# Optimization experiments

Measured on AMD Instinct MI355X. Metric: run time of the kernel, lower is better.

## Reference

```python
import jax, jax.numpy as jnp
import numpy as np

HIDDEN = 256
DEPTH = 3
MOL_ATOMS = 42  # padding_final_size in MPNEncoder.padding (AM_dim0=False)
ATOM_FDIM = 133
BOND_FDIM = 147
N_MOLS = 4000
N_ATOMS = N_MOLS * MOL_ATOMS
N_BONDS = 360000
MAX_NB = 6


def setup_inputs() -> dict:
    key = jax.random.key(0)
    ks = jax.random.split(key, 9)
    f_atoms = jax.random.normal(ks[0], (N_ATOMS, ATOM_FDIM), dtype=jnp.float32)
    f_bonds = jax.random.normal(ks[1], (N_BONDS, BOND_FDIM), dtype=jnp.float32)
    a2b = jax.random.randint(ks[2], (N_ATOMS, MAX_NB), 0, N_BONDS, dtype=jnp.int32)
    b2a = jax.random.randint(ks[3], (N_BONDS,), 0, N_ATOMS, dtype=jnp.int32)
    b2revb = jax.random.randint(ks[4], (N_BONDS,), 0, N_BONDS, dtype=jnp.int32)
    # learned params (bias=False for W_i/W_h, W_o has bias, per chemprop defaults)
    W_i = jax.random.normal(ks[5], (HIDDEN, BOND_FDIM), dtype=jnp.float32) * 0.05
    W_h = jax.random.normal(ks[6], (HIDDEN, HIDDEN), dtype=jnp.float32) * 0.05
    W_o = jax.random.normal(ks[7], (HIDDEN, ATOM_FDIM + HIDDEN), dtype=jnp.float32) * 0.05
    b_o = jax.random.normal(ks[8], (HIDDEN,), dtype=jnp.float32) * 0.05
    return dict(f_atoms=f_atoms, f_bonds=f_bonds, W_i=W_i, W_h=W_h, W_o=W_o,
                b_o=b_o, a2b=a2b, b2a=b2a, b2revb=b2revb)


def reference(f_atoms, f_bonds, W_i, W_h, W_o, b_o, a2b, b2a, b2revb):
    # bond-message MPN (atom_messages=False, undirected=False, dropout=0)
    relu = jax.nn.relu
    inp = f_bonds @ W_i.T                         # [n_bonds, H]
    message = relu(inp)

    def atom_hidden(a_msg):
        a_input = jnp.concatenate([f_atoms, a_msg], axis=1)  # [n_atoms, fa+H]
        return relu(a_input @ W_o.T + b_o)

    # depth-0 hidden: a_input = [f_atoms, zeros(H)] (the 'padding' tensor)
    save_depth = [atom_hidden(jnp.zeros((f_atoms.shape[0], HIDDEN), f_atoms.dtype))]
    for d in range(DEPTH - 1):
        if d == 0:
            save_depth.append(atom_hidden(message[a2b].sum(axis=1)))
        a_message = message[a2b].sum(axis=1)      # gather+sum over neighbors
        message = a_message[b2a] - message[b2revb]
        message = relu(inp + message @ W_h.T)
        save_depth.append(atom_hidden(message[a2b].sum(axis=1)))

    # every molecule has exactly MOL_ATOMS atoms -> padding() is identity,
    # per-molecule narrow/stack becomes a reshape
    def pool(h):
        return h.reshape(N_MOLS, MOL_ATOMS, HIDDEN)

    d0, d1, d2 = pool(save_depth[0]), pool(save_depth[1]), pool(save_depth[2])
    dfin = pool(save_depth[-1])
    mol_vecs = dfin.mean(axis=1)                  # sum / a_size
    return (d0, d1, d2, dfin, mol_vecs)
```

## Files before the change

kernel.cpp:

```cpp
#include <hip/hip_runtime.h>

typedef unsigned short u16;
typedef unsigned int u32;
typedef __bf16 bf16x8 __attribute__((ext_vector_type(8)));
typedef float f32x4 __attribute__((ext_vector_type(4)));

__device__ __forceinline__ float bf2f(u16 h) {
  union { u32 u; float f; } c; c.u = ((u32)h) << 16; return c.f;
}
__device__ __forceinline__ float bflo(u32 u) {
  union { u32 u; float f; } c; c.u = u << 16; return c.f;
}
__device__ __forceinline__ float bfhi(u32 u) {
  union { u32 u; float f; } c; c.u = u & 0xffff0000u; return c.f;
}
__device__ __forceinline__ u32 pack2bf(float a, float b) {
  union { __bf16 h[2]; u32 u; } c; c.h[0] = (__bf16)a; c.h[1] = (__bf16)b;
  return c.u;
}
__device__ __forceinline__ u16 f2bf(float f) {
  union { __bf16 h; u16 u; } c; c.h = (__bf16)f; return c.u;
}
__device__ __forceinline__ float relu(float x) { return x > 0.f ? x : 0.f; }

__global__ __launch_bounds__(256) void cvt_w(const float* __restrict__ src,
                                             u16* __restrict__ dst, int N,
                                             int Ks, int Kd, int src_stride,
                                             int col0) {
  int i = blockIdx.x * 256 + threadIdx.x;
  if (i >= N * Kd) return;
  int n = i / Kd, k = i % Kd;
  float v = (k < Ks) ? src[(size_t)n * src_stride + col0 + k] : 0.f;
  dst[i] = f2bf(v);
}

template <int ASRC, int EPI, int KPAD>
__global__ __launch_bounds__(256, 3) void gemm5(
    const float* __restrict__ Af, int Kreal,
    const u16* __restrict__ Ab, const u16* __restrict__ Ab2,
    const int* __restrict__ idx1, const int* __restrict__ idx2,
    const u16* __restrict__ Bw,
    const u16* __restrict__ addb, const float* __restrict__ bias,
    u16* __restrict__ outb0, float* __restrict__ outf) {
  constexpr int LDK = KPAD + 8;
  __shared__ u16 As[64 * LDK];

  const int tid = threadIdx.x;
  const int lane = tid & 63;
  const int wn = (tid >> 6) * 64;
  const int m0 = blockIdx.x * 64;
  const int lm = lane & 15, lg = lane >> 4;
  const int koff = lg * 8;

  if constexpr (ASRC == 0) {
#pragma unroll
    for (int p = 0; p < 64 * KPAD / 512; ++p) {
      int e = (p * 256 + tid) * 2;
      int row = e / KPAD, k = e % KPAD;
      const float* src = Af + (size_t)(m0 + row) * Kreal + k;
      float x0 = (k < Kreal) ? src[0] : 0.f;
      float x1 = (k + 1 < Kreal) ? src[1] : 0.f;
      *reinterpret_cast<u32*>(&As[row * LDK + k]) = pack2bf(x0, x1);
    }
  } else if constexpr (ASRC == 1) {
#pragma unroll
    for (int p = 0; p < 64 * KPAD / 8 / 256; ++p) {
      int ch = p * 256 + tid;
      int row = ch / (KPAD / 8), c8 = ch % (KPAD / 8);
      uint4 v = *reinterpret_cast<const uint4*>(Ab + (size_t)(m0 + row) * KPAD + c8 * 8);
      *reinterpret_cast<uint4*>(&As[row * LDK + c8 * 8]) = v;
    }
  } else {
    static_assert(KPAD == 256, "ASRC2 assumes KPAD=256");
    const int row = tid >> 2, seg = tid & 3;
    const int gr = m0 + row;
    const int r1 = idx1[gr], r2 = idx2[gr];
    const u16* pa = Ab + (size_t)r1 * KPAD + seg * 64;
    const u16* pb = Ab2 + (size_t)r2 * KPAD + seg * 64;
    uint4 va[8], vb[8];
#pragma unroll
    for (int i = 0; i < 8; ++i) va[i] = *reinterpret_cast<const uint4*>(pa + i * 8);
#pragma unroll
    for (int i = 0; i < 8; ++i) vb[i] = *reinterpret_cast<const uint4*>(pb + i * 8);
    u16* dst = &As[row * LDK + seg * 64];
#pragma unroll
    for (int i = 0; i < 8; ++i) {
      uint4 o;
      o.x = pack2bf(bflo(va[i].x) - relu(bflo(vb[i].x)),
                    bfhi(va[i].x) - relu(bfhi(vb[i].x)));
      o.y = pack2bf(bflo(va[i].y) - relu(bflo(vb[i].y)),
                    bfhi(va[i].y) - relu(bfhi(vb[i].y)));
      o.z = pack2bf(bflo(va[i].z) - relu(bflo(vb[i].z)),
                    bfhi(va[i].z) - relu(bfhi(vb[i].z)));
      o.w = pack2bf(bflo(va[i].w) - relu(bflo(vb[i].w)),
                    bfhi(va[i].w) - relu(bfhi(vb[i].w)));
      *reinterpret_cast<uint4*>(dst + i * 8) = o;
    }
  }
  __syncthreads();

  f32x4 acc[4][4];
#pragma unroll
  for (int i = 0; i < 4; ++i)
#pragma unroll
    for (int j = 0; j < 4; ++j) acc[i][j] = (f32x4)(0.f);

#pragma unroll
  for (int kk = 0; kk < KPAD / 32; ++kk) {
    const int k0 = kk * 32 + koff;
    bf16x8 a[4];
#pragma unroll
    for (int im = 0; im < 4; ++im)
      a[im] = *reinterpret_cast<const bf16x8*>(&As[(im * 16 + lm) * LDK + k0]);
#pragma unroll
    for (int jw = 0; jw < 4; ++jw) {
      bf16x8 b = *reinterpret_cast<const bf16x8*>(
          Bw + (size_t)(wn + jw * 16 + lm) * KPAD + k0);
#pragma unroll
      for (int im = 0; im < 4; ++im)
        acc[im][jw] = __builtin_amdgcn_mfma_f32_16x16x32_bf16(b, a[im], acc[im][jw], 0, 0, 0);
    }
  }

#pragma unroll
  for (int im = 0; im < 4; ++im) {
#pragma unroll
    for (int jw = 0; jw < 4; ++jw) {
      const int r = m0 + im * 16 + lm;
      const int c0 = wn + jw * 16 + lg * 4;
      const size_t idx = (size_t)r * 256 + c0;
      f32x4 v = acc[im][jw];
      if constexpr (EPI == 0) {
        uint2 o; o.x = pack2bf(v[0], v[1]); o.y = pack2bf(v[2], v[3]);
        *reinterpret_cast<uint2*>(outb0 + idx) = o;
      } else if constexpr (EPI == 1) {
        const float4 bb = *reinterpret_cast<const float4*>(bias + c0);
        v[0] += bb.x; v[1] += bb.y; v[2] += bb.z; v[3] += bb.w;
        uint2 o; o.x = pack2bf(v[0], v[1]); o.y = pack2bf(v[2], v[3]);
        *reinterpret_cast<uint2*>(outb0 + idx) = o;
        float4 rl = {relu(v[0]), relu(v[1]), relu(v[2]), relu(v[3])};
        *reinterpret_cast<float4*>(outf + idx) = rl;
      } else if constexpr (EPI == 2) {
        const uint2 ab = *reinterpret_cast<const uint2*>(addb + idx);
        v[0] += bflo(ab.x); v[1] += bfhi(ab.x);
        v[2] += bflo(ab.y); v[3] += bfhi(ab.y);
        uint2 o; o.x = pack2bf(v[0], v[1]); o.y = pack2bf(v[2], v[3]);
        *reinterpret_cast<uint2*>(outb0 + idx) = o;
      } else {
        const uint2 ab = *reinterpret_cast<const uint2*>(addb + idx);
        v[0] += bflo(ab.x); v[1] += bfhi(ab.x);
        v[2] += bflo(ab.y); v[3] += bfhi(ab.y);
        float4 rl = {relu(v[0]), relu(v[1]), relu(v[2]), relu(v[3])};
        *reinterpret_cast<float4*>(outf + idx) = rl;
      }
    }
  }
}

__global__ __launch_bounds__(256) void gather_sum(const u16* __restrict__ S,
                                                  const int* __restrict__ a2b,
                                                  u16* __restrict__ amsg,
                                                  int n_atoms) {
  int wave = threadIdx.x >> 6, lane = threadIdx.x & 63;
  int atom = blockIdx.x * 4 + wave;
  if (atom >= n_atoms) return;
  float s0 = 0.f, s1 = 0.f, s2 = 0.f, s3 = 0.f;
  int base = atom * 6;
#pragma unroll
  for (int j = 0; j < 6; ++j) {
    int b = a2b[base + j];
    ushort4 v = *reinterpret_cast<const ushort4*>(S + (size_t)b * 256 + lane * 4);
    s0 += relu(bf2f(v.x));
    s1 += relu(bf2f(v.y));
    s2 += relu(bf2f(v.z));
    s3 += relu(bf2f(v.w));
  }
  uint2 o;
  o.x = pack2bf(s0, s1);
  o.y = pack2bf(s2, s3);
  *reinterpret_cast<uint2*>(amsg + (size_t)atom * 256 + lane * 4) = o;
}

__global__ __launch_bounds__(256) void mol_mean(const float* __restrict__ dfin,
                                                float* __restrict__ out) {
  int mol = blockIdx.x, c = threadIdx.x;
  const float* p = dfin + (size_t)mol * (42 * 256) + c;
  float s = 0.f;
#pragma unroll
  for (int a = 0; a < 42; ++a) s += p[a * 256];
  out[(size_t)mol * 256 + c] = s * (1.0f / 42.0f);
}

extern "C" void kernel_launch(void* const* d_in, const int* in_sizes, int n_in,
                              void* d_out, int out_size, void* d_ws,
                              size_t ws_size, hipStream_t stream) {
  const float* f_atoms = (const float*)d_in[0];
  const float* f_bonds = (const float*)d_in[1];
  const float* W_i = (const float*)d_in[2];
  const float* W_h = (const float*)d_in[3];
  const float* W_o = (const float*)d_in[4];
  const float* b_o = (const float*)d_in[5];
  const int* a2b = (const int*)d_in[6];
  const int* b2a = (const int*)d_in[7];
  const int* b2revb = (const int*)d_in[8];

  const int NA = 168000, NB = 360000, H = 256;
  const size_t SZ_BH = (size_t)NB * H * 2;
  const size_t SZ_AH = (size_t)NA * H * 2;

  char* ws = (char*)d_ws;
  u16* inp_b = (u16*)ws;  ws += SZ_BH;
  u16* P0    = (u16*)ws;  ws += SZ_BH;
  u16* P1    = (u16*)ws;  ws += SZ_BH;
  u16* amsg  = (u16*)ws;  ws += SZ_AH;
  u16* base_b = (u16*)ws; ws += SZ_AH;
  u16* Wi_b  = (u16*)ws;  ws += 256 * 160 * 2;
  u16* Wh_b  = (u16*)ws;  ws += 256 * 256 * 2;
  u16* Wo1_b = (u16*)ws;  ws += 256 * 160 * 2;
  u16* Wo2_b = (u16*)ws;  ws += 256 * 256 * 2;

  float* out = (float*)d_out;
  float* d0 = out;
  float* d1 = d0 + (size_t)NA * H;
  float* d2 = d1 + (size_t)NA * H;
  float* dfin = d2 + (size_t)NA * H;
  float* mol = dfin + (size_t)NA * H;

  dim3 blk(256);
  cvt_w<<<dim3((256 * 160 + 255) / 256), blk, 0, stream>>>(W_i, Wi_b, 256, 147, 160, 147, 0);
  cvt_w<<<dim3((256 * 256 + 255) / 256), blk, 0, stream>>>(W_h, Wh_b, 256, 256, 256, 256, 0);
  cvt_w<<<dim3((256 * 160 + 255) / 256), blk, 0, stream>>>(W_o, Wo1_b, 256, 133, 160, 389, 0);
  cvt_w<<<dim3((256 * 256 + 255) / 256), blk, 0, stream>>>(W_o, Wo2_b, 256, 256, 256, 389, 133);

  gemm5<0, 0, 160><<<dim3(NB / 64), blk, 0, stream>>>(
      f_bonds, 147, nullptr, nullptr, nullptr, nullptr, Wi_b,
      nullptr, nullptr, inp_b, nullptr);
  gemm5<0, 1, 160><<<dim3(NA / 64), blk, 0, stream>>>(
      f_atoms, 133, nullptr, nullptr, nullptr, nullptr, Wo1_b,
      nullptr, b_o, base_b, d0);

  u16* S = inp_b;
  u16* pms[2] = {P0, P1};
  float* douts[3] = {d1, d2, dfin};
  for (int d = 0; d < 3; ++d) {
    gather_sum<<<dim3(NA / 4), blk, 0, stream>>>(S, a2b, amsg, NA);
    gemm5<1, 3, 256><<<dim3(NA / 64), blk, 0, stream>>>(
        nullptr, 0, amsg, nullptr, nullptr, nullptr, Wo2_b,
        base_b, nullptr, nullptr, douts[d]);
    if (d < 2) {
      gemm5<2, 2, 256><<<dim3(NB / 64), blk, 0, stream>>>(
          nullptr, 0, amsg, S, b2a, b2revb, Wh_b,
          inp_b, nullptr, pms[d], nullptr);
      S = pms[d];
    }
  }
  mol_mean<<<dim3(4000), blk, 0, stream>>>(dfin, mol);
}
```

Measured before the change: 1.553 ms.

## Fuse neighbor gather-sum into atom-output GEMM A-tile load

Removes the separate gather_sum kernel and performs the a2b neighbor gather, relu and sum directly while building the A tile of the atom-output GEMM. On the first two depths the fused kernel also writes amsg to global memory so the bond-update GEMM can still read it. The last depth skips that write. This saves three kernel launches and one amsg write plus re-read per depth. In exchange, each thread holds 32 float accumulators, which adds register pressure. Launch-bounds minimum waves is also raised to 4 for several GEMM variants.

After: 1.474 ms. -5.1%, faster.

```diff
diff --git a/kernel.cpp b/kernel.cpp
--- a/kernel.cpp
+++ b/kernel.cpp
@@ -34,14 +34,15 @@
   dst[i] = f2bf(v);
 }
 
-template <int ASRC, int EPI, int KPAD>
-__global__ __launch_bounds__(256, 3) void gemm5(
+template <int ASRC, int EPI, int KPAD, int WAMSG, int MINW>
+__global__ __launch_bounds__(256, MINW) void gemm6(
     const float* __restrict__ Af, int Kreal,
     const u16* __restrict__ Ab, const u16* __restrict__ Ab2,
     const int* __restrict__ idx1, const int* __restrict__ idx2,
     const u16* __restrict__ Bw,
     const u16* __restrict__ addb, const float* __restrict__ bias,
-    u16* __restrict__ outb0, float* __restrict__ outf) {
+    u16* __restrict__ outb0, float* __restrict__ outf,
+    u16* __restrict__ amsg_out) {
   constexpr int LDK = KPAD + 8;
   __shared__ u16 As[64 * LDK];
 
@@ -70,7 +71,7 @@
       uint4 v = *reinterpret_cast<const uint4*>(Ab + (size_t)(m0 + row) * KPAD + c8 * 8);
       *reinterpret_cast<uint4*>(&As[row * LDK + c8 * 8]) = v;
     }
-  } else {
+  } else if constexpr (ASRC == 2) {
     static_assert(KPAD == 256, "ASRC2 assumes KPAD=256");
     const int row = tid >> 2, seg = tid & 3;
     const int gr = m0 + row;
@@ -95,6 +96,45 @@
       o.w = pack2bf(bflo(va[i].w) - relu(bflo(vb[i].w)),
                     bfhi(va[i].w) - relu(bfhi(vb[i].w)));
       *reinterpret_cast<uint4*>(dst + i * 8) = o;
+    }
+  } else {
+    static_assert(KPAD == 256, "ASRC3 assumes KPAD=256");
+#pragma unroll
+    for (int pass = 0; pass < 2; ++pass) {
+      const int row = pass * 32 + (tid >> 3);
+      const int seg = tid & 7;
+      const int gr = m0 + row;
+      const int* nb = idx1 + gr * 6;
+      float s[32];
+#pragma unroll
+      for (int e = 0; e < 32; ++e) s[e] = 0.f;
+      for (int j = 0; j < 6; ++j) {
+        const u16* p = Ab + (size_t)nb[j] * 256 + seg * 32;
+#pragma unroll
+        for (int c = 0; c < 4; ++c) {
+          uint4 v = *reinterpret_cast<const uint4*>(p + c * 8);
+          s[c * 8 + 0] += relu(bflo(v.x));
+          s[c * 8 + 1] += relu(bfhi(v.x));
+          s[c * 8 + 2] += relu(bflo(v.y));
+          s[c * 8 + 3] += relu(bfhi(v.y));
+          s[c * 8 + 4] += relu(bflo(v.z));
+          s[c * 8 + 5] += relu(bfhi(v.z));
+          s[c * 8 + 6] += relu(bflo(v.w));
+          s[c * 8 + 7] += relu(bfhi(v.w));
+        }
+      }
+      u16* dst = &As[row * LDK + seg * 32];
+#pragma unroll
+      for (int c = 0; c < 4; ++c) {
+        uint4 o;
+        o.x = pack2bf(s[c * 8 + 0], s[c * 8 + 1]);
+        o.y = pack2bf(s[c * 8 + 2], s[c * 8 + 3]);
+        o.z = pack2bf(s[c * 8 + 4], s[c * 8 + 5]);
+        o.w = pack2bf(s[c * 8 + 6], s[c * 8 + 7]);
+        *reinterpret_cast<uint4*>(dst + c * 8) = o;
+        if constexpr (WAMSG)
+          *reinterpret_cast<uint4*>(amsg_out + (size_t)gr * 256 + seg * 32 + c * 8) = o;
+      }
     }
   }
   __syncthreads();
@@ -157,30 +197,6 @@
   }
 }
 
-__global__ __launch_bounds__(256) void gather_sum(const u16* __restrict__ S,
-                                                  const int* __restrict__ a2b,
-                                                  u16* __restrict__ amsg,
-                                                  int n_atoms) {
-  int wave = threadIdx.x >> 6, lane = threadIdx.x & 63;
-  int atom = blockIdx.x * 4 + wave;
-  if (atom >= n_atoms) return;
-  float s0 = 0.f, s1 = 0.f, s2 = 0.f, s3 = 0.f;
-  int base = atom * 6;
-#pragma unroll
-  for (int j = 0; j < 6; ++j) {
-    int b = a2b[base + j];
-    ushort4 v = *reinterpret_cast<const ushort4*>(S + (size_t)b * 256 + lane * 4);
-    s0 += relu(bf2f(v.x));
-    s1 += relu(bf2f(v.y));
-    s2 += relu(bf2f(v.z));
-    s3 += relu(bf2f(v.w));
-  }
-  uint2 o;
-  o.x = pack2bf(s0, s1);
-  o.y = pack2bf(s2, s3);
-  *reinterpret_cast<uint2*>(amsg + (size_t)atom * 256 + lane * 4) = o;
-}
-
 __global__ __launch_bounds__(256) void mol_mean(const float* __restrict__ dfin,
                                                 float* __restrict__ out) {
   int mol = blockIdx.x, c = threadIdx.x;
@@ -232,26 +248,29 @@
   cvt_w<<<dim3((256 * 160 + 255) / 256), blk, 0, stream>>>(W_o, Wo1_b, 256, 133, 160, 389, 0);
   cvt_w<<<dim3((256 * 256 + 255) / 256), blk, 0, stream>>>(W_o, Wo2_b, 256, 256, 256, 389, 133);
 
-  gemm5<0, 0, 160><<<dim3(NB / 64), blk, 0, stream>>>(
+  gemm6<0, 0, 160, 0, 4><<<dim3(NB / 64), blk, 0, stream>>>(
       f_bonds, 147, nullptr, nullptr, nullptr, nullptr, Wi_b,
-      nullptr, nullptr, inp_b, nullptr);
-  gemm5<0, 1, 160><<<dim3(NA / 64), blk, 0, stream>>>(
+      nullptr, nullptr, inp_b, nullptr, nullptr);
+  gemm6<0, 1, 160, 0, 4><<<dim3(NA / 64), blk, 0, stream>>>(
       f_atoms, 133, nullptr, nullptr, nullptr, nullptr, Wo1_b,
-      nullptr, b_o, base_b, d0);
+      nullptr, b_o, base_b, d0, nullptr);
 
   u16* S = inp_b;
   u16* pms[2] = {P0, P1};
   float* douts[3] = {d1, d2, dfin};
   for (int d = 0; d < 3; ++d) {
-    gather_sum<<<dim3(NA / 4), blk, 0, stream>>>(S, a2b, amsg, NA);
-    gemm5<1, 3, 256><<<dim3(NA / 64), blk, 0, stream>>>(
-        nullptr, 0, amsg, nullptr, nullptr, nullptr, Wo2_b,
-        base_b, nullptr, nullptr, douts[d]);
     if (d < 2) {
-      gemm5<2, 2, 256><<<dim3(NB / 64), blk, 0, stream>>>(
+      gemm6<3, 3, 256, 1, 4><<<dim3(NA / 64), blk, 0, stream>>>(
+          nullptr, 0, S, nullptr, a2b, nullptr, Wo2_b,
+          base_b, nullptr, nullptr, douts[d], amsg);
+      gemm6<2, 2, 256, 0, 3><<<dim3(NB / 64), blk, 0, stream>>>(
           nullptr, 0, amsg, S, b2a, b2revb, Wh_b,
-          inp_b, nullptr, pms[d], nullptr);
+          inp_b, nullptr, pms[d], nullptr, nullptr);
       S = pms[d];
+    } else {
+      gemm6<3, 3, 256, 0, 4><<<dim3(NA / 64), blk, 0, stream>>>(
+          nullptr, 0, S, nullptr, a2b, nullptr, Wo2_b,
+          base_b, nullptr, nullptr, douts[d], nullptr);
     }
   }
   mol_mean<<<dim3(4000), blk, 0, stream>>>(dfin, mol);
```
